# Kernel optimization log

Hardware: AMD Instinct MI355X
Metric: run time of the kernel (lower is better)

The kernel has to match this reference:

```python
import jax, jax.numpy as jnp
import numpy as np

# Model dims (match init_kwargs)
D_MODEL = 1024
D_INNER = 2048
D_STATE = 16
D_CONV = 4
DT_RANK = 64
H = 8                      # num_heads
P = D_INNER // H           # head_dim = 256
DT_MIN, DT_MAX = 1e-4, 1.0
BATCH, SEQ = 2, 4096
TOTAL_OUT = 2 * D_INNER + DT_RANK + 2 * H * D_STATE  # 4416 (no gated delta)
EPS = 1e-6


def _xavier(k, shape):
    fan_out, fan_in = shape
    return jax.random.normal(k, shape, jnp.float32) * np.sqrt(2.0 / (fan_in + fan_out))


def setup_inputs() -> dict:
    key = jax.random.key(0)
    ks = jax.random.split(key, 8)
    x = jax.random.normal(ks[0], (BATCH, SEQ, D_MODEL), jnp.float32)
    W_in = _xavier(ks[1], (TOTAL_OUT, D_MODEL))          # in_proj (no bias)
    W_dt = _xavier(ks[2], (H, DT_RANK))                  # dt_proj (no bias)
    conv_w = jax.random.normal(ks[3], (D_INNER, D_CONV), jnp.float32) * 0.1
    conv_b = jnp.zeros((D_INNER,), jnp.float32)
    # A_log init: log(1..d_state) per head
    A_log = jnp.broadcast_to(jnp.log(jnp.arange(1, D_STATE + 1, dtype=jnp.float32)), (H, D_STATE))
    Dskip = jnp.ones((H, P), jnp.float32)
    # dt_bias = inverse_softplus(dt), dt log-uniform in [dt_min, dt_max]
    dt0 = jnp.exp(jax.random.uniform(ks[4], (H,), jnp.float32)
                  * (np.log(DT_MAX) - np.log(DT_MIN)) + np.log(DT_MIN))
    dt_bias = dt0 + jnp.log(-jnp.expm1(-dt0))
    norm_w = jnp.ones((D_INNER,), jnp.float32)
    W_out = _xavier(ks[5], (D_MODEL, D_INNER))
    W_res = _xavier(ks[6], (D_INNER, D_MODEL))           # residual_proj (d_model != d_inner)
    return dict(x=x, W_in=W_in, W_dt=W_dt, conv_w=conv_w, conv_b=conv_b,
                A_log=A_log, Dskip=Dskip, dt_bias=dt_bias, norm_w=norm_w,
                W_out=W_out, W_res=W_res)


def _causal_dwconv(u, w, b):
    # u: (B,L,C) -> causal depthwise conv along L. w: (C,K), b: (C,)
    lhs = u.transpose(0, 2, 1)               # (B,C,L)
    rhs = w[:, None, :]                      # (C,1,K)
    out = jax.lax.conv_general_dilated(
        lhs, rhs, window_strides=(1,), padding=[(D_CONV - 1, 0)],
        dimension_numbers=('NCH', 'OIH', 'NCH'), feature_group_count=D_INNER)
    return (out + b[None, :, None]).transpose(0, 2, 1)


def reference(x, W_in, W_dt, conv_w, conv_b, A_log, Dskip, dt_bias, norm_w, W_out, W_res):
    Bsz, L, _ = x.shape
    p = x @ W_in.T                                            # (B,L,TOTAL_OUT)
    splits = np.cumsum([D_INNER, D_INNER, DT_RANK, H * D_STATE]).tolist()
    z, u, dt_h, Bf, Cf = jnp.split(p, splits, axis=-1)
    Bp = Bf.reshape(Bsz, L, H, D_STATE)
    Cp = Cf.reshape(Bsz, L, H, D_STATE)
    u = _causal_dwconv(u, conv_w, conv_b)                     # (B,L,D_INNER)
    # dt_prep: softplus(dt_raw + bias) clamped to [dt_min, dt_max]
    dt = jnp.clip(jax.nn.softplus(dt_h @ W_dt.T + dt_bias), DT_MIN, DT_MAX)  # (B,L,H)
    A = -jnp.exp(A_log)                                       # (H,N)
    uh = u.reshape(Bsz, L, H, P)

    def step(h, inp):
        u_t, dt_t, B_t, C_t = inp                             # (B,H,P),(B,H),(B,H,N),(B,H,N)
        dA = jnp.exp(dt_t[..., None] * A)                     # (B,H,N)
        h = h * dA[:, :, None, :] + (dt_t[:, :, None, None] * u_t[..., None]) * B_t[:, :, None, :]
        y_t = jnp.einsum('bhpn,bhn->bhp', h, C_t)
        return h, y_t

    h0 = jnp.zeros((Bsz, H, P, D_STATE), x.dtype)
    xs = (uh.transpose(1, 0, 2, 3), dt.transpose(1, 0, 2),
          Bp.transpose(1, 0, 2, 3), Cp.transpose(1, 0, 2, 3))
    _, ys = jax.lax.scan(step, h0, xs)                        # (L,B,H,P)
    y = ys.transpose(1, 0, 2, 3) + Dskip[None, None] * uh     # skip connection
    y = y.reshape(Bsz, L, D_INNER)

    residual_inner = x @ W_res.T                              # residual_proj
    # fused_out: g = RMSNorm(y * silu(z) + residual) * weight
    g = y * jax.nn.silu(z) + residual_inner
    g = g * jax.lax.rsqrt(jnp.mean(g * g, axis=-1, keepdims=True) + EPS) * norm_w
    return g @ W_out.T
```

## Files before the change

### kernel.cpp

```cpp
#include <hip/hip_runtime.h>
#include <hip/hip_bf16.h>
#include <math.h>

#define DMODEL  1024
#define DINNER  2048
#define DSTATE  16
#define DCONV   4
#define DTRANK  64
#define NH      8
#define PH      256
#define TOTOUT  4416
#define NPAD    4480
#define MB_ROWS 4096
#define LC      64
#define NCB     (MB_ROWS/LC)

typedef __attribute__((ext_vector_type(8))) short bf16x8;
typedef __attribute__((ext_vector_type(4))) float f32x4;

__device__ inline unsigned cvt2bf(float lo, float hi) {
    unsigned r;
    asm("v_cvt_pk_bf16_f32 %0, %1, %2" : "=v"(r) : "v"(lo), "v"(hi));
    return r;
}
__device__ inline ushort f2bf(float v) { return (ushort)(cvt2bf(v, v) & 0xffffu); }
__device__ inline float bf2f(ushort u) {
    union { unsigned u; float f; } w; w.u = (unsigned)u << 16; return w.f;
}
__device__ inline void gload16(const ushort* g, ushort* l) {
    __builtin_amdgcn_global_load_lds((const __attribute__((address_space(1))) unsigned*)(const void*)g,
                                     (__attribute__((address_space(3))) unsigned*)(void*)l, 16, 0, 0);
}

__global__ __launch_bounds__(256) void cvt_bf(const float* __restrict__ s,
                                              ushort* __restrict__ d) {
    size_t i = ((size_t)blockIdx.x * 256 + threadIdx.x) * 8;
    float4 v0 = *(const float4*)(s + i);
    float4 v1 = *(const float4*)(s + i + 4);
    uint4 o;
    o.x = cvt2bf(v0.x, v0.y); o.y = cvt2bf(v0.z, v0.w);
    o.z = cvt2bf(v1.x, v1.y); o.w = cvt2bf(v1.z, v1.w);
    *(uint4*)(d + i) = o;
}

__global__ __launch_bounds__(256) void cvt_weights(const float* __restrict__ W_in,
                                                   const float* __restrict__ W_res,
                                                   const float* __restrict__ W_out,
                                                   ushort* __restrict__ dst) {
    const size_t R0v = (size_t)TOTOUT * DMODEL;
    const size_t R0  = (size_t)NPAD * DMODEL;
    const size_t R1  = R0 + (size_t)DINNER * DMODEL;
    size_t i = ((size_t)blockIdx.x * 256 + threadIdx.x) * 8;
    float4 v0, v1;
    if (i < R0) {
        if (i < R0v) { v0 = *(const float4*)(W_in + i); v1 = *(const float4*)(W_in + i + 4); }
        else { v0 = make_float4(0.f,0.f,0.f,0.f); v1 = v0; }
    } else if (i < R1) {
        size_t o = i - R0; v0 = *(const float4*)(W_res + o); v1 = *(const float4*)(W_res + o + 4);
    } else {
        size_t o = i - R1; v0 = *(const float4*)(W_out + o); v1 = *(const float4*)(W_out + o + 4);
    }
    uint4 o;
    o.x = cvt2bf(v0.x, v0.y); o.y = cvt2bf(v0.z, v0.w);
    o.z = cvt2bf(v1.x, v1.y); o.w = cvt2bf(v1.z, v1.w);
    *(uint4*)(dst + i) = o;
}

template<int MODE>
__global__ __launch_bounds__(256) void gemm_bf16(const ushort* __restrict__ A,
                                                 const ushort* __restrict__ W,
                                                 float* __restrict__ C0,
                                                 ushort* __restrict__ Zb,
                                                 ushort* __restrict__ Ub,
                                                 float* __restrict__ DBCp,
                                                 int ntx, int K, int ldc) {
    __shared__ __align__(16) ushort Al[2][128 * 32];
    __shared__ __align__(16) ushort Bl[2][128 * 32];
    const int nwg  = gridDim.x;
    const int orig = blockIdx.x;
    const int swz  = (orig & 7) * (nwg >> 3) + (orig >> 3);
    const int bx = swz % ntx, by = swz / ntx;
    const int row0 = by * 128, col0 = bx * 128;

    const int t    = threadIdx.x;
    const int lane = t & 63, w = t >> 6;
    const int wr   = w >> 1, wc = w & 1;
    const int l15  = lane & 15, l4 = lane >> 4;

    const int gr = t >> 2, gk = (t & 3) * 8;
    const ushort* Ag  = A + (size_t)(row0 + gr) * K + gk;
    const ushort* Ag2 = Ag + (size_t)64 * K;
    const ushort* Wg  = W + (size_t)(col0 + gr) * K + gk;
    const ushort* Wg2 = Wg + (size_t)64 * K;

    f32x4 acc[4][4];
    #pragma unroll
    for (int i = 0; i < 4; i++)
        #pragma unroll
        for (int j = 0; j < 4; j++)
            acc[i][j] = (f32x4){0.f, 0.f, 0.f, 0.f};

    gload16(Ag,  &Al[0][t * 8]);
    gload16(Ag2, &Al[0][2048 + t * 8]);
    gload16(Wg,  &Bl[0][t * 8]);
    gload16(Wg2, &Bl[0][2048 + t * 8]);
    __syncthreads();

    const int KT = K >> 5;
    for (int kt = 0; kt < KT; ++kt) {
        const int cur = kt & 1;
        if (kt + 1 < KT) {
            const int ko = (kt + 1) << 5;
            gload16(Ag + ko,  &Al[cur ^ 1][t * 8]);
            gload16(Ag2 + ko, &Al[cur ^ 1][2048 + t * 8]);
            gload16(Wg + ko,  &Bl[cur ^ 1][t * 8]);
            gload16(Wg2 + ko, &Bl[cur ^ 1][2048 + t * 8]);
        }
        const bf16x8* Av = (const bf16x8*)Al[cur];
        const bf16x8* Bv = (const bf16x8*)Bl[cur];
        bf16x8 af[4], bw[4];
        #pragma unroll
        for (int mi = 0; mi < 4; mi++)
            af[mi] = Av[(wr * 64 + mi * 16 + l15) * 4 + l4];
        #pragma unroll
        for (int ni = 0; ni < 4; ni++)
            bw[ni] = Bv[(wc * 64 + ni * 16 + l15) * 4 + l4];
        #pragma unroll
        for (int mi = 0; mi < 4; mi++)
            #pragma unroll
            for (int ni = 0; ni < 4; ni++)
                acc[mi][ni] = __builtin_amdgcn_mfma_f32_16x16x32_bf16(af[mi], bw[ni], acc[mi][ni], 0, 0, 0);
        __syncthreads();
    }

    #pragma unroll
    for (int mi = 0; mi < 4; mi++) {
        #pragma unroll
        for (int ni = 0; ni < 4; ni++) {
            #pragma unroll
            for (int r = 0; r < 4; r++) {
                const int row = row0 + wr * 64 + mi * 16 + l4 * 4 + r;
                const int col = col0 + wc * 64 + ni * 16 + l15;
                const float v = acc[mi][ni][r];
                if (MODE == 0) {
                    C0[(size_t)row * ldc + col] = v;
                } else if (MODE == 1) {
                    C0[(size_t)row * ldc + col] += v;
                } else {
                    if (col0 < DINNER) {
                        Zb[(size_t)row * DINNER + col] = f2bf(v);
                    } else if (col0 < 2 * DINNER) {
                        Ub[(size_t)row * DINNER + (col - DINNER)] = f2bf(v);
                    } else if (col < TOTOUT) {
                        DBCp[(size_t)row * 320 + (col - 2 * DINNER)] = v;
                    }
                }
            }
        }
    }
}

__global__ __launch_bounds__(256) void dt_kernel(const float* __restrict__ DBC,
                                                 const float* __restrict__ W_dt,
                                                 const float* __restrict__ dt_bias,
                                                 const float* __restrict__ A_log,
                                                 float* __restrict__ dt,
                                                 float* __restrict__ dA) {
    int idx = blockIdx.x * blockDim.x + threadIdx.x;
    int h = idx % NH;
    int tr = idx / NH;
    const float* row = DBC + (size_t)tr * 320;
    float acc = dt_bias[h];
    #pragma unroll
    for (int r = 0; r < DTRANK; r++) acc = fmaf(row[r], W_dt[h * DTRANK + r], acc);
    float sp = acc > 20.f ? acc : log1pf(expf(acc));
    sp = fminf(fmaxf(sp, 1e-4f), 1.0f);
    dt[idx] = sp;
    #pragma unroll
    for (int n = 0; n < DSTATE; n++)
        dA[(size_t)idx * DSTATE + n] = expf(sp * (-expf(A_log[h * DSTATE + n])));
}

__global__ __launch_bounds__(256) void scan_local(const ushort* __restrict__ Ub,
                                                  const float* __restrict__ DBC,
                                                  const float* __restrict__ dt_,
                                                  const float* __restrict__ dA_,
                                                  const float* __restrict__ cw,
                                                  const float* __restrict__ cb,
                                                  float* __restrict__ hloc,
                                                  float* __restrict__ Pc) {
    const int c = blockIdx.x, h = blockIdx.y;
    const int pidx = threadIdx.x;
    const int ch = h * PH + pidx;
    const int t0 = c * LC;
    __shared__ float sdA[LC][DSTATE];
    __shared__ float sdB[LC][DSTATE];
    const int st = pidx >> 4, sn = pidx & 15;
    #pragma unroll
    for (int j = 0; j < 4; j++) {
        int tt = st + j * 16;
        size_t trow = (size_t)(t0 + tt);
        float dv = dt_[trow * NH + h];
        sdA[tt][sn] = dA_[(trow * NH + h) * DSTATE + sn];
        sdB[tt][sn] = dv * DBC[trow * 320 + 64 + h * DSTATE + sn];
    }
    const float w0 = cw[ch * 4], w1 = cw[ch * 4 + 1], w2 = cw[ch * 4 + 2], w3 = cw[ch * 4 + 3];
    const float bia = cb[ch];
    const int bs = (c / NCB) * MB_ROWS;
    float um3 = (t0 - 3 >= bs) ? bf2f(Ub[(size_t)(t0 - 3) * DINNER + ch]) : 0.f;
    float um2 = (t0 - 2 >= bs) ? bf2f(Ub[(size_t)(t0 - 2) * DINNER + ch]) : 0.f;
    float um1 = (t0 - 1 >= bs) ? bf2f(Ub[(size_t)(t0 - 1) * DINNER + ch]) : 0.f;
    __syncthreads();

    float hst[DSTATE] = {};
    for (int t = 0; t < LC; t++) {
        float u0 = bf2f(Ub[(size_t)(t0 + t) * DINNER + ch]);
        float up = fmaf(w3, u0, fmaf(w2, um1, fmaf(w1, um2, fmaf(w0, um3, bia))));
        um3 = um2; um2 = um1; um1 = u0;
        #pragma unroll
        for (int n = 0; n < DSTATE; n++)
            hst[n] = fmaf(hst[n], sdA[t][n], up * sdB[t][n]);
    }
    float* hl = hloc + (((size_t)c * NH + h) * PH + pidx) * DSTATE;
    #pragma unroll
    for (int n = 0; n < DSTATE; n++) hl[n] = hst[n];

    if (pidx < DSTATE) {
        float pr = 1.f;
        for (int t = 0; t < LC; t++) pr *= sdA[t][pidx];
        Pc[((size_t)c * NH + h) * DSTATE + pidx] = pr;
    }
}

__global__ __launch_bounds__(256) void scan_carry(const float* __restrict__ hloc,
                                                  const float* __restrict__ Pc,
                                                  float* __restrict__ Hent) {
    int g = blockIdx.x * 256 + threadIdx.x;
    int b = g >> 15;
    int r = g & 32767;
    int h = r >> 12;
    int inner = r & 4095;
    int n = r & 15;
    float carry = 0.f;
    for (int i = 0; i < NCB; i++) {
        int c = b * NCB + i;
        size_t idx = ((size_t)c * NH + h) * (PH * DSTATE) + inner;
        Hent[idx] = carry;
        carry = fmaf(Pc[((size_t)c * NH + h) * DSTATE + n], carry, hloc[idx]);
    }
}

__global__ __launch_bounds__(256) void scan_out(const ushort* __restrict__ Zb,
                                                const ushort* __restrict__ Ub,
                                                float* __restrict__ UC,
                                                const float* __restrict__ DBC,
                                                const float* __restrict__ dt_,
                                                const float* __restrict__ dA_,
                                                const float* __restrict__ cw,
                                                const float* __restrict__ cb,
                                                const float* __restrict__ Dskip,
                                                const float* __restrict__ Hent) {
    const int c = blockIdx.x, h = blockIdx.y;
    const int pidx = threadIdx.x;
    const int ch = h * PH + pidx;
    const int t0 = c * LC;
    __shared__ float sdA[LC][DSTATE];
    __shared__ float sdB[LC][DSTATE];
    __shared__ float sC [LC][DSTATE];
    const int st = pidx >> 4, sn = pidx & 15;
    #pragma unroll
    for (int j = 0; j < 4; j++) {
        int tt = st + j * 16;
        size_t trow = (size_t)(t0 + tt);
        float dv = dt_[trow * NH + h];
        sdA[tt][sn] = dA_[(trow * NH + h) * DSTATE + sn];
        sdB[tt][sn] = dv * DBC[trow * 320 + 64 + h * DSTATE + sn];
        sC [tt][sn] =      DBC[trow * 320 + 192 + h * DSTATE + sn];
    }
    const float w0 = cw[ch * 4], w1 = cw[ch * 4 + 1], w2 = cw[ch * 4 + 2], w3 = cw[ch * 4 + 3];
    const float bia = cb[ch];
    const int bs = (c / NCB) * MB_ROWS;
    float um3 = (t0 - 3 >= bs) ? bf2f(Ub[(size_t)(t0 - 3) * DINNER + ch]) : 0.f;
    float um2 = (t0 - 2 >= bs) ? bf2f(Ub[(size_t)(t0 - 2) * DINNER + ch]) : 0.f;
    float um1 = (t0 - 1 >= bs) ? bf2f(Ub[(size_t)(t0 - 1) * DINNER + ch]) : 0.f;
    const float dsk = Dskip[ch];
    float hst[DSTATE];
    const float* he = Hent + (((size_t)c * NH + h) * PH + pidx) * DSTATE;
    #pragma unroll
    for (int n = 0; n < DSTATE; n++) hst[n] = he[n];
    __syncthreads();

    for (int t = 0; t < LC; t++) {
        size_t off = (size_t)(t0 + t) * DINNER + ch;
        float u0 = bf2f(Ub[off]);
        float up = fmaf(w3, u0, fmaf(w2, um1, fmaf(w1, um2, fmaf(w0, um3, bia))));
        um3 = um2; um2 = um1; um1 = u0;
        float a0 = 0.f, a1 = 0.f, a2 = 0.f, a3 = 0.f;
        #pragma unroll
        for (int n = 0; n < 4; n++) {
            hst[n +  0] = fmaf(hst[n +  0], sdA[t][n +  0], up * sdB[t][n +  0]);
            hst[n +  4] = fmaf(hst[n +  4], sdA[t][n +  4], up * sdB[t][n +  4]);
            hst[n +  8] = fmaf(hst[n +  8], sdA[t][n +  8], up * sdB[t][n +  8]);
            hst[n + 12] = fmaf(hst[n + 12], sdA[t][n + 12], up * sdB[t][n + 12]);
            a0 = fmaf(hst[n +  0], sC[t][n +  0], a0);
            a1 = fmaf(hst[n +  4], sC[t][n +  4], a1);
            a2 = fmaf(hst[n +  8], sC[t][n +  8], a2);
            a3 = fmaf(hst[n + 12], sC[t][n + 12], a3);
        }
        float yv = ((a0 + a1) + (a2 + a3)) + dsk * up;
        float zv = bf2f(Zb[off]);
        float sil = zv / (1.f + expf(-zv));
        UC[off] = yv * sil;
    }
}

__global__ __launch_bounds__(256) void rmsnorm_bf(const float* __restrict__ G,
                                                  const float* __restrict__ norm_w,
                                                  ushort* __restrict__ Gb) {
    const int row = blockIdx.x;
    const float* r = G + (size_t)row * DINNER;
    const int c0 = threadIdx.x * 8;
    float4 v0 = *(const float4*)(r + c0);
    float4 v1 = *(const float4*)(r + c0 + 4);
    float ss = v0.x * v0.x;
    ss = fmaf(v0.y, v0.y, ss); ss = fmaf(v0.z, v0.z, ss); ss = fmaf(v0.w, v0.w, ss);
    ss = fmaf(v1.x, v1.x, ss); ss = fmaf(v1.y, v1.y, ss);
    ss = fmaf(v1.z, v1.z, ss); ss = fmaf(v1.w, v1.w, ss);
    #pragma unroll
    for (int off = 32; off > 0; off >>= 1) ss += __shfl_down(ss, off);
    __shared__ float red[4];
    if ((threadIdx.x & 63) == 0) red[threadIdx.x >> 6] = ss;
    __syncthreads();
    float tot = red[0] + red[1] + red[2] + red[3];
    float inv = rsqrtf(tot / (float)DINNER + 1e-6f);
    float4 w0 = *(const float4*)(norm_w + c0);
    float4 w1 = *(const float4*)(norm_w + c0 + 4);
    uint4 o;
    o.x = cvt2bf(v0.x * inv * w0.x, v0.y * inv * w0.y);
    o.y = cvt2bf(v0.z * inv * w0.z, v0.w * inv * w0.w);
    o.z = cvt2bf(v1.x * inv * w1.x, v1.y * inv * w1.y);
    o.w = cvt2bf(v1.z * inv * w1.z, v1.w * inv * w1.w);
    *(uint4*)(Gb + (size_t)row * DINNER + c0) = o;
}

struct Lay {
    float *UC, *DBC, *DT, *DA, *PC, *HLOC, *HENT;
    ushort *ZB, *UB, *XBF, *WB;
    size_t total;
};
static Lay mk_layout(char* base, int Mr) {
    size_t o = 0;
    auto take = [&](size_t bytes) { char* p = base + o; o = (o + bytes + 255) & ~(size_t)255; return p; };
    Lay l;
    l.UC   = (float*) take((size_t)Mr * 2048 * 4);
    l.DBC  = (float*) take((size_t)Mr * 320 * 4);
    l.DT   = (float*) take((size_t)Mr * 8 * 4);
    l.DA   = (float*) take((size_t)Mr * 128 * 4);
    l.PC   = (float*) take((size_t)(Mr / 64) * NH * DSTATE * 4);
    l.HLOC = (float*) take((size_t)Mr * 512 * 4);
    l.HENT = (float*) take((size_t)Mr * 512 * 4);
    l.ZB   = (ushort*)take((size_t)Mr * 2048 * 2);
    l.UB   = (ushort*)take((size_t)Mr * 2048 * 2);
    l.XBF  = (ushort*)take((size_t)8192 * 1024 * 2);
    l.WB   = (ushort*)take(((size_t)NPAD * 1024 + (size_t)2048 * 1024 + (size_t)1024 * 2048) * 2);
    l.total = o;
    return l;
}

extern "C" void kernel_launch(void* const* d_in, const int* in_sizes, int n_in,
                              void* d_out, int out_size, void* d_ws, size_t ws_size,
                              hipStream_t stream) {
    const float* x       = (const float*)d_in[0];
    const float* W_in    = (const float*)d_in[1];
    const float* W_dt    = (const float*)d_in[2];
    const float* conv_w  = (const float*)d_in[3];
    const float* conv_b  = (const float*)d_in[4];
    const float* A_log   = (const float*)d_in[5];
    const float* Dskip   = (const float*)d_in[6];
    const float* dt_bias = (const float*)d_in[7];
    const float* norm_w  = (const float*)d_in[8];
    const float* W_out   = (const float*)d_in[9];
    const float* W_res   = (const float*)d_in[10];
    float* out = (float*)d_out;

    Lay probe = mk_layout(nullptr, 2 * MB_ROWS);
    const bool fat = ws_size >= probe.total;
    const int Mr = fat ? 2 * MB_ROWS : MB_ROWS;
    const int npass = fat ? 1 : 2;
    const int nbc = fat ? 2 : 1;
    Lay l = mk_layout((char*)d_ws, Mr);

    ushort* winb = l.WB;
    ushort* wrsb = winb + (size_t)NPAD * 1024;
    ushort* wotb = wrsb + (size_t)2048 * 1024;
    ushort* Gb   = l.ZB;

    cvt_weights<<<4288, 256, 0, stream>>>(W_in, W_res, W_out, l.WB);
    cvt_bf<<<(2 * MB_ROWS * DMODEL / 8) / 256, 256, 0, stream>>>(x, l.XBF);

    const int NT = Mr / 128;
    for (int b = 0; b < npass; b++) {
        const ushort* xb = l.XBF + (size_t)b * MB_ROWS * DMODEL;
        float* outb = out + (size_t)b * MB_ROWS * DMODEL;

        gemm_bf16<2><<<35 * NT, 256, 0, stream>>>(xb, winb, nullptr, l.ZB, l.UB, l.DBC, 35, DMODEL, 0);
        dt_kernel<<<(Mr * NH) / 256, 256, 0, stream>>>(l.DBC, W_dt, dt_bias, A_log, l.DT, l.DA);
        scan_local<<<dim3(Mr / LC, NH), 256, 0, stream>>>(l.UB, l.DBC, l.DT, l.DA, conv_w, conv_b, l.HLOC, l.PC);
        scan_carry<<<nbc * 128, 256, 0, stream>>>(l.HLOC, l.PC, l.HENT);
        scan_out<<<dim3(Mr / LC, NH), 256, 0, stream>>>(l.ZB, l.UB, l.UC, l.DBC, l.DT, l.DA,
                                                        conv_w, conv_b, Dskip, l.HENT);
        gemm_bf16<1><<<16 * NT, 256, 0, stream>>>(xb, wrsb, l.UC, nullptr, nullptr, nullptr, 16, DMODEL, DINNER);
        rmsnorm_bf<<<Mr, 256, 0, stream>>>(l.UC, norm_w, Gb);
        gemm_bf16<0><<<8 * NT, 256, 0, stream>>>(Gb, wotb, outb, nullptr, nullptr, nullptr, 8, DINNER, DMODEL);
    }
}
```

Measured before the change: 369.9 us.

## Triple-buffer swizzled 256x128 GEMM tiles and store y*silu(z) intermediate as bf16

The bf16 GEMM is rebuilt with 512-thread blocks covering 256x128 output tiles. It uses a three-stage LDS ring with XOR-swizzled addresses, waits on explicit vmcnt with raw barriers, and raises wave priority around the MFMA block. The y*silu(z) intermediate and the residual accumulation now use bf16 instead of fp32, which halves that buffer's traffic in scan_out, the residual GEMM and rmsnorm. In exchange, the pre-norm activations are rounded to bf16 before the residual add and the norm, which adds precision loss.

```diff
diff --git a/kernel.cpp b/kernel.cpp
--- a/kernel.cpp
+++ b/kernel.cpp
@@ -67,31 +67,45 @@
 }
 
 template<int MODE>
-__global__ __launch_bounds__(256) void gemm_bf16(const ushort* __restrict__ A,
-                                                 const ushort* __restrict__ W,
-                                                 float* __restrict__ C0,
-                                                 ushort* __restrict__ Zb,
-                                                 ushort* __restrict__ Ub,
-                                                 float* __restrict__ DBCp,
-                                                 int ntx, int K, int ldc) {
-    __shared__ __align__(16) ushort Al[2][128 * 32];
-    __shared__ __align__(16) ushort Bl[2][128 * 32];
+__global__ __launch_bounds__(512) void gemm_p(const ushort* __restrict__ A,
+                                              const ushort* __restrict__ W,
+                                              float* __restrict__ C0,
+                                              ushort* __restrict__ Cb,
+                                              ushort* __restrict__ Zb,
+                                              ushort* __restrict__ Ub,
+                                              float* __restrict__ DBCp,
+                                              int ntx, int K, int ldc) {
+    __shared__ __align__(16) ushort L[3 * 12288];
     const int nwg  = gridDim.x;
     const int orig = blockIdx.x;
     const int swz  = (orig & 7) * (nwg >> 3) + (orig >> 3);
     const int bx = swz % ntx, by = swz / ntx;
-    const int row0 = by * 128, col0 = bx * 128;
+    const int row0 = by * 256, col0 = bx * 128;
 
     const int t    = threadIdx.x;
     const int lane = t & 63, w = t >> 6;
     const int wr   = w >> 1, wc = w & 1;
     const int l15  = lane & 15, l4 = lane >> 4;
 
-    const int gr = t >> 2, gk = (t & 3) * 8;
-    const ushort* Ag  = A + (size_t)(row0 + gr) * K + gk;
-    const ushort* Ag2 = Ag + (size_t)64 * K;
-    const ushort* Wg  = W + (size_t)(col0 + gr) * K + gk;
-    const ushort* Wg2 = Wg + (size_t)64 * K;
+    const int r0g = t >> 2, s0g = t & 3;
+    const int r1g = r0g + 128;
+    const int rr0 = r0g ^ ((r0g >> 3) & 1), cc0 = s0g ^ ((r0g >> 1) & 3);
+    const int rr1 = r1g ^ ((r1g >> 3) & 1), cc1 = s0g ^ ((r1g >> 1) & 3);
+    const ushort* sA0 = A + (size_t)(row0 + rr0) * K + cc0 * 8;
+    const ushort* sA1 = A + (size_t)(row0 + rr1) * K + cc1 * 8;
+    const ushort* sB0 = W + (size_t)(col0 + rr0) * K + cc0 * 8;
+
+    int offA[4], offB[4];
+    #pragma unroll
+    for (int mi = 0; mi < 4; mi++) {
+        int r = wr * 64 + mi * 16 + l15;
+        offA[mi] = (r * 32 + l4 * 8) ^ (((r >> 1) & 7) << 3);
+    }
+    #pragma unroll
+    for (int ni = 0; ni < 4; ni++) {
+        int r = wc * 64 + ni * 16 + l15;
+        offB[ni] = 8192 + ((r * 32 + l4 * 8) ^ (((r >> 1) & 7) << 3));
+    }
 
     f32x4 acc[4][4];
     #pragma unroll
@@ -100,37 +114,47 @@
         for (int j = 0; j < 4; j++)
             acc[i][j] = (f32x4){0.f, 0.f, 0.f, 0.f};
 
-    gload16(Ag,  &Al[0][t * 8]);
-    gload16(Ag2, &Al[0][2048 + t * 8]);
-    gload16(Wg,  &Bl[0][t * 8]);
-    gload16(Wg2, &Bl[0][2048 + t * 8]);
-    __syncthreads();
-
     const int KT = K >> 5;
+    {
+        gload16(sA0,      &L[t * 8]);
+        gload16(sA1,      &L[4096 + t * 8]);
+        gload16(sB0,      &L[8192 + t * 8]);
+        gload16(sA0 + 32, &L[12288 + t * 8]);
+        gload16(sA1 + 32, &L[12288 + 4096 + t * 8]);
+        gload16(sB0 + 32, &L[12288 + 8192 + t * 8]);
+    }
+    asm volatile("s_waitcnt vmcnt(3)" ::: "memory");
+    __builtin_amdgcn_sched_barrier(0);
+    __builtin_amdgcn_s_barrier();
+    __builtin_amdgcn_sched_barrier(0);
+
     for (int kt = 0; kt < KT; ++kt) {
-        const int cur = kt & 1;
-        if (kt + 1 < KT) {
-            const int ko = (kt + 1) << 5;
-            gload16(Ag + ko,  &Al[cur ^ 1][t * 8]);
-            gload16(Ag2 + ko, &Al[cur ^ 1][2048 + t * 8]);
-            gload16(Wg + ko,  &Bl[cur ^ 1][t * 8]);
-            gload16(Wg2 + ko, &Bl[cur ^ 1][2048 + t * 8]);
+        const bool pre = (kt + 2) < KT;
+        if (pre) {
+            ushort* bp2 = &L[((kt + 2) % 3) * 12288];
+            const int ko = (kt + 2) << 5;
+            gload16(sA0 + ko, bp2 + t * 8);
+            gload16(sA1 + ko, bp2 + 4096 + t * 8);
+            gload16(sB0 + ko, bp2 + 8192 + t * 8);
         }
-        const bf16x8* Av = (const bf16x8*)Al[cur];
-        const bf16x8* Bv = (const bf16x8*)Bl[cur];
+        const ushort* bp = &L[(kt % 3) * 12288];
         bf16x8 af[4], bw[4];
         #pragma unroll
-        for (int mi = 0; mi < 4; mi++)
-            af[mi] = Av[(wr * 64 + mi * 16 + l15) * 4 + l4];
-        #pragma unroll
-        for (int ni = 0; ni < 4; ni++)
-            bw[ni] = Bv[(wc * 64 + ni * 16 + l15) * 4 + l4];
+        for (int mi = 0; mi < 4; mi++) af[mi] = *(const bf16x8*)(bp + offA[mi]);
+        #pragma unroll
+        for (int ni = 0; ni < 4; ni++) bw[ni] = *(const bf16x8*)(bp + offB[ni]);
+        __builtin_amdgcn_s_setprio(1);
         #pragma unroll
         for (int mi = 0; mi < 4; mi++)
             #pragma unroll
             for (int ni = 0; ni < 4; ni++)
                 acc[mi][ni] = __builtin_amdgcn_mfma_f32_16x16x32_bf16(af[mi], bw[ni], acc[mi][ni], 0, 0, 0);
-        __syncthreads();
+        __builtin_amdgcn_s_setprio(0);
+        if (pre) { asm volatile("s_waitcnt vmcnt(3)" ::: "memory"); }
+        else     { asm volatile("s_waitcnt vmcnt(0)" ::: "memory"); }
+        __builtin_amdgcn_sched_barrier(0);
+        __builtin_amdgcn_s_barrier();
+        __builtin_amdgcn_sched_barrier(0);
     }
 
     #pragma unroll
@@ -145,7 +169,8 @@
                 if (MODE == 0) {
                     C0[(size_t)row * ldc + col] = v;
                 } else if (MODE == 1) {
-                    C0[(size_t)row * ldc + col] += v;
+                    size_t idx = (size_t)row * ldc + col;
+                    Cb[idx] = f2bf(bf2f(Cb[idx]) + v);
                 } else {
                     if (col0 < DINNER) {
                         Zb[(size_t)row * DINNER + col] = f2bf(v);
@@ -252,7 +277,7 @@
 
 __global__ __launch_bounds__(256) void scan_out(const ushort* __restrict__ Zb,
                                                 const ushort* __restrict__ Ub,
-                                                float* __restrict__ UC,
+                                                ushort* __restrict__ Yb,
                                                 const float* __restrict__ DBC,
                                                 const float* __restrict__ dt_,
                                                 const float* __restrict__ dA_,
@@ -310,22 +335,25 @@
         float yv = ((a0 + a1) + (a2 + a3)) + dsk * up;
         float zv = bf2f(Zb[off]);
         float sil = zv / (1.f + expf(-zv));
-        UC[off] = yv * sil;
-    }
-}
-
-__global__ __launch_bounds__(256) void rmsnorm_bf(const float* __restrict__ G,
+        Yb[off] = f2bf(yv * sil);
+    }
+}
+
+__global__ __launch_bounds__(256) void rmsnorm_bf(const ushort* __restrict__ Yb,
                                                   const float* __restrict__ norm_w,
                                                   ushort* __restrict__ Gb) {
     const int row = blockIdx.x;
-    const float* r = G + (size_t)row * DINNER;
+    const ushort* r = Yb + (size_t)row * DINNER;
     const int c0 = threadIdx.x * 8;
-    float4 v0 = *(const float4*)(r + c0);
-    float4 v1 = *(const float4*)(r + c0 + 4);
-    float ss = v0.x * v0.x;
-    ss = fmaf(v0.y, v0.y, ss); ss = fmaf(v0.z, v0.z, ss); ss = fmaf(v0.w, v0.w, ss);
-    ss = fmaf(v1.x, v1.x, ss); ss = fmaf(v1.y, v1.y, ss);
-    ss = fmaf(v1.z, v1.z, ss); ss = fmaf(v1.w, v1.w, ss);
+    uint4 packed = *(const uint4*)(r + c0);
+    float v[8];
+    v[0] = bf2f((ushort)(packed.x & 0xffff)); v[1] = bf2f((ushort)(packed.x >> 16));
+    v[2] = bf2f((ushort)(packed.y & 0xffff)); v[3] = bf2f((ushort)(packed.y >> 16));
+    v[4] = bf2f((ushort)(packed.z & 0xffff)); v[5] = bf2f((ushort)(packed.z >> 16));
+    v[6] = bf2f((ushort)(packed.w & 0xffff)); v[7] = bf2f((ushort)(packed.w >> 16));
+    float ss = 0.f;
+    #pragma unroll
+    for (int i = 0; i < 8; i++) ss = fmaf(v[i], v[i], ss);
     #pragma unroll
     for (int off = 32; off > 0; off >>= 1) ss += __shfl_down(ss, off);
     __shared__ float red[4];
@@ -336,23 +364,23 @@
     float4 w0 = *(const float4*)(norm_w + c0);
     float4 w1 = *(const float4*)(norm_w + c0 + 4);
     uint4 o;
-    o.x = cvt2bf(v0.x * inv * w0.x, v0.y * inv * w0.y);
-    o.y = cvt2bf(v0.z * inv * w0.z, v0.w * inv * w0.w);
-    o.z = cvt2bf(v1.x * inv * w1.x, v1.y * inv * w1.y);
-    o.w = cvt2bf(v1.z * inv * w1.z, v1.w * inv * w1.w);
+    o.x = cvt2bf(v[0] * inv * w0.x, v[1] * inv * w0.y);
+    o.y = cvt2bf(v[2] * inv * w0.z, v[3] * inv * w0.w);
+    o.z = cvt2bf(v[4] * inv * w1.x, v[5] * inv * w1.y);
+    o.w = cvt2bf(v[6] * inv * w1.z, v[7] * inv * w1.w);
     *(uint4*)(Gb + (size_t)row * DINNER + c0) = o;
 }
 
 struct Lay {
-    float *UC, *DBC, *DT, *DA, *PC, *HLOC, *HENT;
-    ushort *ZB, *UB, *XBF, *WB;
+    float *DBC, *DT, *DA, *PC, *HLOC, *HENT;
+    ushort *YB, *ZB, *UB, *XBF, *WB;
     size_t total;
 };
 static Lay mk_layout(char* base, int Mr) {
     size_t o = 0;
     auto take = [&](size_t bytes) { char* p = base + o; o = (o + bytes + 255) & ~(size_t)255; return p; };
     Lay l;
-    l.UC   = (float*) take((size_t)Mr * 2048 * 4);
+    l.YB   = (ushort*)take((size_t)Mr * 2048 * 2);
     l.DBC  = (float*) take((size_t)Mr * 320 * 4);
     l.DT   = (float*) take((size_t)Mr * 8 * 4);
     l.DA   = (float*) take((size_t)Mr * 128 * 4);
@@ -398,19 +426,19 @@
     cvt_weights<<<4288, 256, 0, stream>>>(W_in, W_res, W_out, l.WB);
     cvt_bf<<<(2 * MB_ROWS * DMODEL / 8) / 256, 256, 0, stream>>>(x, l.XBF);
 
-    const int NT = Mr / 128;
     for (int b = 0; b < npass; b++) {
         const ushort* xb = l.XBF + (size_t)b * MB_ROWS * DMODEL;
         float* outb = out + (size_t)b * MB_ROWS * DMODEL;
-
-        gemm_bf16<2><<<35 * NT, 256, 0, stream>>>(xb, winb, nullptr, l.ZB, l.UB, l.DBC, 35, DMODEL, 0);
+        const int nty = Mr / 256;
+
+        gemm_p<2><<<35 * nty, 512, 0, stream>>>(xb, winb, nullptr, nullptr, l.ZB, l.UB, l.DBC, 35, DMODEL, 0);
         dt_kernel<<<(Mr * NH) / 256, 256, 0, stream>>>(l.DBC, W_dt, dt_bias, A_log, l.DT, l.DA);
         scan_local<<<dim3(Mr / LC, NH), 256, 0, stream>>>(l.UB, l.DBC, l.DT, l.DA, conv_w, conv_b, l.HLOC, l.PC);
         scan_carry<<<nbc * 128, 256, 0, stream>>>(l.HLOC, l.PC, l.HENT);
-        scan_out<<<dim3(Mr / LC, NH), 256, 0, stream>>>(l.ZB, l.UB, l.UC, l.DBC, l.DT, l.DA,
+        scan_out<<<dim3(Mr / LC, NH), 256, 0, stream>>>(l.ZB, l.UB, l.YB, l.DBC, l.DT, l.DA,
                                                         conv_w, conv_b, Dskip, l.HENT);
-        gemm_bf16<1><<<16 * NT, 256, 0, stream>>>(xb, wrsb, l.UC, nullptr, nullptr, nullptr, 16, DMODEL, DINNER);
-        rmsnorm_bf<<<Mr, 256, 0, stream>>>(l.UC, norm_w, Gb);
-        gemm_bf16<0><<<8 * NT, 256, 0, stream>>>(Gb, wotb, outb, nullptr, nullptr, nullptr, 8, DINNER, DMODEL);
-    }
-}
+        gemm_p<1><<<16 * nty, 512, 0, stream>>>(xb, wrsb, nullptr, l.YB, nullptr, nullptr, nullptr, 16, DMODEL, DINNER);
+        rmsnorm_bf<<<Mr, 256, 0, stream>>>(l.YB, norm_w, Gb);
+        gemm_p<0><<<8 * nty, 512, 0, stream>>>(Gb, wotb, outb, nullptr, nullptr, nullptr, nullptr, 8, DINNER, DMODEL);
+    }
+}
```

After: 307.5 us. 16.9% less time.
